# Kernel tuning notes

Hardware: AMD Instinct MI355X
Metric: run time of the kernel (lower is better)

The kernel has to match this reference:

```python
import jax, jax.numpy as jnp
import numpy as np

DIM = 2048
HEADS = 16
DIM_HEAD = 128
INNER = HEADS * DIM_HEAD  # 2048


def rotate_half(x):
    # split last dim into two halves, return cat(-x2, x1)
    x1, x2 = jnp.split(x, 2, axis=-1)
    return jnp.concatenate((-x2, x1), axis=-1)


def rotary_pos(n, dim_head, dtype):
    inv_freq = 1.0 / (10000.0 ** (jnp.arange(0, dim_head, 2, dtype=jnp.float32) / dim_head))
    seq = jnp.arange(n, dtype=jnp.float32)
    freqs = jnp.einsum('i,j->ij', seq, inv_freq)  # [n, dim_head//2]
    return jnp.concatenate((freqs, freqs), axis=-1).astype(dtype)  # [n, dim_head]


def apply_rotary(pos, t):
    return t * jnp.cos(pos) + rotate_half(t) * jnp.sin(pos)


def setup_inputs() -> dict:
    key = jax.random.key(0)
    ks = jax.random.split(key, 9)
    s = 0.02
    return {
        'x': jax.random.normal(ks[0], (2, 2048, DIM), dtype=jnp.float32),
        'Wq': jax.random.normal(ks[1], (DIM, INNER), dtype=jnp.float32) * s,
        'bq': jnp.zeros((INNER,), dtype=jnp.float32),
        'Wk': jax.random.normal(ks[2], (DIM, INNER), dtype=jnp.float32) * s,
        'bk': jnp.zeros((INNER,), dtype=jnp.float32),
        'Wv': jax.random.normal(ks[3], (DIM, INNER), dtype=jnp.float32) * s,
        'bv': jnp.zeros((INNER,), dtype=jnp.float32),
        'Wo': jax.random.normal(ks[4], (INNER, DIM), dtype=jnp.float32) * s,
        'bo': jnp.zeros((DIM,), dtype=jnp.float32),
    }


def reference(x, Wq, bq, Wk, bk, Wv, bv, Wo, bo):
    b, n, _ = x.shape
    scale = DIM_HEAD ** -0.5

    def proj(W, bias):
        t = x @ W + bias                       # [b, n, inner]
        return t.reshape(b, n, HEADS, DIM_HEAD).transpose(0, 2, 1, 3)  # [b, h, n, d]

    q = proj(Wq, bq) * scale
    k = proj(Wk, bk)
    v = proj(Wv, bv)

    pos = rotary_pos(n, DIM_HEAD, x.dtype)     # [n, d]
    q = apply_rotary(pos, q)
    k = apply_rotary(pos, k)

    sim = jnp.einsum('bhid,bhjd->bhij', q, k)  # [b, h, n, n]
    causal = jnp.triu(jnp.ones((n, n), dtype=bool), k=1)
    sim = jnp.where(causal, -jnp.finfo(sim.dtype).max, sim)
    attn = jax.nn.softmax(sim, axis=-1)

    out = jnp.einsum('bhij,bhjd->bhid', attn, v)
    out = out.transpose(0, 2, 1, 3).reshape(b, n, INNER)
    return out @ Wo + bo
```

## Files before the change

kernel.cpp:

```cpp
#include <hip/hip_runtime.h>
#include <stdint.h>

typedef unsigned short u16;
typedef __bf16 bf16x8 __attribute__((ext_vector_type(8)));
typedef float f32x4 __attribute__((ext_vector_type(4)));
typedef float f32x16 __attribute__((ext_vector_type(16)));
typedef unsigned short u16x8 __attribute__((ext_vector_type(8)));
typedef unsigned short u16x4 __attribute__((ext_vector_type(4)));

#define MFMA16(a, b, c) __builtin_amdgcn_mfma_f32_16x16x32_bf16(a, b, c, 0, 0, 0)
#define MFMA32(a, b, c) __builtin_amdgcn_mfma_f32_32x32x16_bf16(a, b, c, 0, 0, 0)

static __device__ __forceinline__ u16 f2bf(float f) {
  union { float f; uint32_t u; } v; v.f = f;
  uint32_t r = 0x7FFFu + ((v.u >> 16) & 1u);
  return (u16)((v.u + r) >> 16);
}
static __device__ __forceinline__ float bf2f(u16 h) {
  union { uint32_t u; float f; } v; v.u = ((uint32_t)h) << 16;
  return v.f;
}

static __device__ __forceinline__ void gld_lds16(const u16* g, u16* l) {
  __builtin_amdgcn_global_load_lds(
      (const __attribute__((address_space(1))) void*)g,
      (__attribute__((address_space(3))) void*)l, 16, 0, 0);
}

__global__ __launch_bounds__(256) void cast_f32_to_bf16(
    const float* __restrict__ in, u16* __restrict__ out, int n4) {
  int i = blockIdx.x * blockDim.x + threadIdx.x;
  if (i >= n4) return;
  const float4 v = ((const float4*)in)[i];
  u16x4 o;
  o[0] = f2bf(v.x); o[1] = f2bf(v.y); o[2] = f2bf(v.z); o[3] = f2bf(v.w);
  ((u16x4*)out)[i] = o;
}

__global__ __launch_bounds__(256) void transpose_cast(
    const float* __restrict__ W, u16* __restrict__ Wt, int R, int C) {
  __shared__ float tile[32][33];
  const int bx = blockIdx.x * 32;
  const int by = blockIdx.y * 32;
  const int tx = threadIdx.x & 31, ty = threadIdx.x >> 5;
#pragma unroll
  for (int i = 0; i < 32; i += 8)
    tile[ty + i][tx] = W[(long)(by + ty + i) * C + bx + tx];
  __syncthreads();
#pragma unroll
  for (int i = 0; i < 32; i += 8)
    Wt[(long)(bx + ty + i) * R + by + tx] = f2bf(tile[tx][ty + i]);
}

__global__ __launch_bounds__(256) void rope_kernel(
    u16* __restrict__ q, u16* __restrict__ k) {
  const int idx = blockIdx.x * blockDim.x + threadIdx.x;
  if (idx >= 4096 * 16 * 64) return;
  const int j = idx & 63;
  const int h = (idx >> 6) & 15;
  const int row = idx >> 10;
  const int npos = row & 2047;
  const float inv_freq = exp2f(-0.20762051f * (float)j);
  const float pos = (float)npos * inv_freq;
  float s, c;
  sincosf(pos, &s, &c);
  const float scale = 0.08838834764831845f;
  const long base = (long)row * 2048 + h * 128 + j;
  float q1 = bf2f(q[base]), q2 = bf2f(q[base + 64]);
  q[base]      = f2bf((q1 * c - q2 * s) * scale);
  q[base + 64] = f2bf((q2 * c + q1 * s) * scale);
  float k1 = bf2f(k[base]), k2 = bf2f(k[base + 64]);
  k[base]      = f2bf(k1 * c - k2 * s);
  k[base + 64] = f2bf(k2 * c + k1 * s);
}

template <int OUT_F32>
static __device__ __forceinline__ void gemm_tile(
    const u16* __restrict__ A, const u16* __restrict__ Bt,
    const float* __restrict__ bias, void* __restrict__ C,
    const int M, const int N, const int K,
    u16* As, u16* Bs, const int bx, const int by) {
  const int tid = threadIdx.x;
  const int wave = tid >> 6;
  const int lane = tid & 63;
  const int lr = lane & 15, hi = lane >> 4;
  const int row0 = by * 128, col0 = bx * 128;
  const int wr = (wave >> 1) * 64, wc = (wave & 1) * 64;

  const int srow = tid >> 2;
  const int scol = (tid & 3) * 8;
  const u16* gA0 = A + (long)(row0 + srow) * K + scol;
  const u16* gA1 = gA0 + (long)64 * K;
  const u16* gB0 = Bt + (long)(col0 + srow) * K + scol;
  const u16* gB1 = gB0 + (long)64 * K;
  u16* lA0 = As + wave * 512;
  u16* lA1 = As + 2048 + wave * 512;
  u16* lB0 = Bs + wave * 512;
  u16* lB1 = Bs + 2048 + wave * 512;

  f32x4 acc[4][4] = {};

  for (int k0 = 0; k0 < K; k0 += 32) {
    __syncthreads();
    gld_lds16(gA0 + k0, lA0);
    gld_lds16(gA1 + k0, lA1);
    gld_lds16(gB0 + k0, lB0);
    gld_lds16(gB1 + k0, lB1);
    __syncthreads();
    bf16x8 af[4], bfr[4];
#pragma unroll
    for (int m = 0; m < 4; ++m)
      af[m] = *(const bf16x8*)&As[(wr + m * 16 + lr) * 32 + hi * 8];
#pragma unroll
    for (int n = 0; n < 4; ++n)
      bfr[n] = *(const bf16x8*)&Bs[(wc + n * 16 + lr) * 32 + hi * 8];
#pragma unroll
    for (int m = 0; m < 4; ++m)
#pragma unroll
      for (int n = 0; n < 4; ++n)
        acc[m][n] = MFMA16(af[m], bfr[n], acc[m][n]);
  }

#pragma unroll
  for (int n = 0; n < 4; ++n) {
    const int gcol = col0 + wc + n * 16 + lr;
    const float bb = bias[gcol];
#pragma unroll
    for (int m = 0; m < 4; ++m) {
      const int grow = row0 + wr + m * 16 + 4 * hi;
#pragma unroll
      for (int i = 0; i < 4; ++i) {
        const float v = acc[m][n][i] + bb;
        if (OUT_F32)
          ((float*)C)[(long)(grow + i) * N + gcol] = v;
        else
          ((u16*)C)[(long)(grow + i) * N + gcol] = f2bf(v);
      }
    }
  }
}

__global__ __launch_bounds__(256, 2) void gemm_qkv_kernel(
    const u16* __restrict__ xb,
    const u16* __restrict__ wtq, const u16* __restrict__ wtk, const u16* __restrict__ wtv,
    const float* __restrict__ bq, const float* __restrict__ bk, const float* __restrict__ bv,
    u16* __restrict__ qo, u16* __restrict__ ko, u16* __restrict__ vo) {
  __shared__ u16 As[4096], Bs[4096];
  const u16* Bt; const float* bias; u16* C;
  if (blockIdx.z == 0)      { Bt = wtq; bias = bq; C = qo; }
  else if (blockIdx.z == 1) { Bt = wtk; bias = bk; C = ko; }
  else                      { Bt = wtv; bias = bv; C = vo; }
  gemm_tile<0>(xb, Bt, bias, C, 4096, 2048, 2048, As, Bs, blockIdx.x, blockIdx.y);
}

__global__ __launch_bounds__(256, 2) void gemm_out_kernel(
    const u16* __restrict__ ao, const u16* __restrict__ wto,
    const float* __restrict__ bo, float* __restrict__ out) {
  __shared__ u16 As[4096], Bs[4096];
  gemm_tile<1>(ao, wto, bo, out, 4096, 2048, 2048, As, Bs, blockIdx.x, blockIdx.y);
}

__global__ __launch_bounds__(256, 2) void flash_attn_kernel(
    const u16* __restrict__ Q, const u16* __restrict__ K,
    const u16* __restrict__ V, u16* __restrict__ O) {
  __shared__ u16 Ks[2][8192];
  __shared__ char Vs[2][16640];

  const int tid = threadIdx.x;
  const int w = tid >> 6;
  const int lane = tid & 63;
  const int l31 = lane & 31, hi5 = lane >> 5, l15 = lane & 15, bit4 = (lane >> 4) & 1;
  const int qt = 15 - blockIdx.x;
  const int q0 = qt * 128;
  const int bh = blockIdx.y;
  const long plane = (long)(bh >> 4) * 2048 * 2048 + (long)(bh & 15) * 128;
  const u16* Qb = Q + plane;
  const u16* Kb = K + plane;
  const u16* Vb = V + plane;
  const int qrow = q0 + w * 32 + l31;

  bf16x8 qf[8];
#pragma unroll
  for (int c = 0; c < 8; ++c)
    qf[c] = *(const bf16x8*)(Qb + (long)qrow * 2048 + c * 16 + hi5 * 8);

  int srcKoff[4], srcVoff[4];
#pragma unroll
  for (int cc = 0; cc < 4; ++cc) {
    const int ci = cc * 256 + tid;
    const int krow = ci >> 4;
    const int cL = (ci & 15) * 16;
    srcKoff[cc] = krow * 2048 + ((cL ^ ((krow & 15) << 4)) >> 1);
    const int dg16 = ci >> 7;
    const int w2 = ci & 127;
    srcVoff[cc] = (w2 >> 1) * 2048 + dg16 * 16 + (w2 & 1) * 8;
  }

  f32x16 ot[4] = {};
  float m = -3e38f, lp = 0.f;
  const int nkt = 2 * qt + 2;
  const int swzk = l15 << 4;
  const int vbase = bit4 * 2080 + hi5 * 256 + l15 * 8;

  auto STAGE = [&](int buf, int kt1) {
    const long koff = (long)kt1 * 131072;
#pragma unroll
    for (int cc = 0; cc < 4; ++cc) {
      gld_lds16(Kb + koff + srcKoff[cc], &Ks[buf][cc * 2048 + w * 512]);
      const int ci0 = cc * 256 + w * 64;
      gld_lds16(Vb + koff + srcVoff[cc],
                (u16*)&Vs[buf][(ci0 >> 7) * 2080 + (ci0 & 127) * 16]);
    }
  };

  STAGE(0, 0);
  for (int kt = 0; kt < nkt; ++kt) {
    __syncthreads();
    if (kt + 1 < nkt) STAGE((kt + 1) & 1, kt + 1);
    const int kv0 = kt * 64;
    if (kv0 > q0 + w * 32 + 31) continue;

    const char* KT = (const char*)Ks[kt & 1];
    const char* VT = Vs[kt & 1];

    f32x16 sa[2] = {};
#pragma unroll
    for (int g = 0; g < 2; ++g) {
      const int rowb = (g * 32 + l31) * 256;
#pragma unroll
      for (int c = 0; c < 8; ++c) {
        const int ab = rowb + ((c * 32 + hi5 * 16) ^ swzk);
        const bf16x8 kf = *(const bf16x8*)(KT + ab);
        sa[g] = MFMA32(kf, qf[c], sa[g]);
      }
    }

    if (kv0 + 63 > q0 + w * 32) {
#pragma unroll
      for (int g = 0; g < 2; ++g)
#pragma unroll
        for (int r = 0; r < 16; ++r) {
          const int kv = kv0 + g * 32 + (r & 3) + 8 * (r >> 2) + 4 * hi5;
          if (kv > qrow) sa[g][r] = -1e30f;
        }
    }

    float pm = -3e38f;
#pragma unroll
    for (int g = 0; g < 2; ++g)
#pragma unroll
      for (int r = 0; r < 16; ++r) pm = fmaxf(pm, sa[g][r]);
    pm = fmaxf(pm, __shfl_xor(pm, 32));
    const float mnew = fmaxf(m, pm);
    const float alpha = __expf(m - mnew);
    float psum = 0.f;
#pragma unroll
    for (int g = 0; g < 2; ++g)
#pragma unroll
      for (int r = 0; r < 16; ++r) {
        const float pv = __expf(sa[g][r] - mnew);
        sa[g][r] = pv;
        psum += pv;
      }
    lp = lp * alpha + psum;
    m = mnew;
#pragma unroll
    for (int dg = 0; dg < 4; ++dg) ot[dg] *= alpha;

    uint32_t pk[2][8];
#pragma unroll
    for (int g = 0; g < 2; ++g)
#pragma unroll
      for (int k2 = 0; k2 < 8; ++k2)
        asm("v_cvt_pk_bf16_f32 %0, %1, %2"
            : "=v"(pk[g][k2]) : "v"(sa[g][2 * k2]), "v"(sa[g][2 * k2 + 1]));

    bf16x8 pfrag[4];
#pragma unroll
    for (int kc = 0; kc < 4; ++kc) {
      const int g = kc >> 1, b = 4 * (kc & 1);
      const uint32_t lo0 = pk[g][b],     lo1 = pk[g][b + 1];
      const uint32_t hh0 = pk[g][b + 2], hh1 = pk[g][b + 3];
      const uint32_t s0v = hi5 ? lo0 : hh0;
      const uint32_t s1v = hi5 ? lo1 : hh1;
      const uint32_t r0 = (uint32_t)__shfl_xor((int)s0v, 32);
      const uint32_t r1 = (uint32_t)__shfl_xor((int)s1v, 32);
      union { uint32_t u[4]; bf16x8 v; } fu;
      fu.u[0] = hi5 ? r0 : lo0;
      fu.u[1] = hi5 ? r1 : lo1;
      fu.u[2] = hi5 ? hh0 : r0;
      fu.u[3] = hi5 ? hh1 : r1;
      pfrag[kc] = fu.v;
    }

#pragma unroll
    for (int dg = 0; dg < 4; ++dg) {
      unsigned long long t[8];
#pragma unroll
      for (int kc = 0; kc < 4; ++kc)
#pragma unroll
        for (int r = 0; r < 2; ++r) {
          const uint32_t a = (uint32_t)(size_t)VT + (uint32_t)(vbase + dg * 4160 + kc * 512 + r * 128);
          asm volatile("ds_read_b64_tr_b16 %0, %1" : "=v"(t[kc * 2 + r]) : "v"(a));
        }
      asm volatile("s_waitcnt lgkmcnt(0)" ::: "memory");
      __builtin_amdgcn_sched_barrier(0);
#pragma unroll
      for (int kc = 0; kc < 4; ++kc) {
        union { unsigned long long q[2]; bf16x8 v; } vu;
        vu.q[0] = t[kc * 2]; vu.q[1] = t[kc * 2 + 1];
        ot[dg] = MFMA32(vu.v, pfrag[kc], ot[dg]);
      }
    }
  }

  const float lt = lp + __shfl_xor(lp, 32);
  const float inv = 1.0f / lt;
  u16* Ob = (u16*)O + plane;
#pragma unroll
  for (int dg = 0; dg < 4; ++dg)
#pragma unroll
    for (int rq = 0; rq < 4; ++rq) {
      u16x4 pk4;
#pragma unroll
      for (int j = 0; j < 4; ++j) pk4[j] = f2bf(ot[dg][rq * 4 + j] * inv);
      *(u16x4*)(Ob + (long)qrow * 2048 + dg * 32 + 8 * rq + 4 * hi5) = pk4;
    }
}

extern "C" void kernel_launch(void* const* d_in, const int* in_sizes, int n_in,
                              void* d_out, int out_size, void* d_ws, size_t ws_size,
                              hipStream_t stream) {
  const float* x  = (const float*)d_in[0];
  const float* Wq = (const float*)d_in[1];
  const float* bq = (const float*)d_in[2];
  const float* Wk = (const float*)d_in[3];
  const float* bk = (const float*)d_in[4];
  const float* Wv = (const float*)d_in[5];
  const float* bv = (const float*)d_in[6];
  const float* Wo = (const float*)d_in[7];
  const float* bo = (const float*)d_in[8];
  float* out = (float*)d_out;

  char* ws = (char*)d_ws;
  size_t off = 0;
  u16* xb   = (u16*)(ws + off); off += (size_t)4096 * 2048 * 2;
  u16* wtq  = (u16*)(ws + off); off += (size_t)2048 * 2048 * 2;
  u16* wtk  = (u16*)(ws + off); off += (size_t)2048 * 2048 * 2;
  u16* wtv  = (u16*)(ws + off); off += (size_t)2048 * 2048 * 2;
  u16* wto  = (u16*)(ws + off); off += (size_t)2048 * 2048 * 2;
  u16* qlin = (u16*)(ws + off); off += (size_t)4096 * 2048 * 2;
  u16* klin = (u16*)(ws + off); off += (size_t)4096 * 2048 * 2;
  u16* vlin = (u16*)(ws + off); off += (size_t)4096 * 2048 * 2;
  u16* aout = (u16*)(ws + off); off += (size_t)4096 * 2048 * 2;
  (void)ws_size; (void)in_sizes; (void)n_in; (void)out_size;

  cast_f32_to_bf16<<<dim3(8192), dim3(256), 0, stream>>>(x, xb, 4096 * 2048 / 4);
  dim3 tgrid(64, 64);
  transpose_cast<<<tgrid, dim3(256), 0, stream>>>(Wq, wtq, 2048, 2048);
  transpose_cast<<<tgrid, dim3(256), 0, stream>>>(Wk, wtk, 2048, 2048);
  transpose_cast<<<tgrid, dim3(256), 0, stream>>>(Wv, wtv, 2048, 2048);
  transpose_cast<<<tgrid, dim3(256), 0, stream>>>(Wo, wto, 2048, 2048);

  gemm_qkv_kernel<<<dim3(16, 32, 3), dim3(256), 0, stream>>>(
      xb, wtq, wtk, wtv, bq, bk, bv, qlin, klin, vlin);
  rope_kernel<<<dim3(16384), dim3(256), 0, stream>>>(qlin, klin);
  flash_attn_kernel<<<dim3(16, 32), dim3(256), 0, stream>>>(qlin, klin, vlin, aout);
  gemm_out_kernel<<<dim3(16, 32), dim3(256), 0, stream>>>(aout, wto, bo, out);
}
```

Measured before the change: 434.5 us.

## Rewrite GEMM tiles as double-buffered 128x256 tiles with swizzled LDS and prefetch

Replaces the single-buffered 128x128, K=32 GEMM tile with a 512-thread 128x256 tile that steps K by 64. Global-to-LDS loads for the next step are issued while the current step's MFMAs run, with explicit vmcnt waits, barriers and setprio hints. The LDS layout is XOR-swizzled to avoid bank conflicts. The goal is to hide global-load latency and raise arithmetic intensity in the QKV and output projections, at the cost of much larger LDS use (96KB per block) and fewer blocks in flight.

```diff
diff --git a/kernel.cpp b/kernel.cpp
--- a/kernel.cpp
+++ b/kernel.cpp
@@ -75,59 +75,115 @@
 }
 
 template <int OUT_F32>
-static __device__ __forceinline__ void gemm_tile(
+static __device__ __forceinline__ void gemm_bigtile(
     const u16* __restrict__ A, const u16* __restrict__ Bt,
     const float* __restrict__ bias, void* __restrict__ C,
-    const int M, const int N, const int K,
     u16* As, u16* Bs, const int bx, const int by) {
+  constexpr int K = 2048, N = 2048;
   const int tid = threadIdx.x;
-  const int wave = tid >> 6;
-  const int lane = tid & 63;
-  const int lr = lane & 15, hi = lane >> 4;
-  const int row0 = by * 128, col0 = bx * 128;
-  const int wr = (wave >> 1) * 64, wc = (wave & 1) * 64;
-
-  const int srow = tid >> 2;
-  const int scol = (tid & 3) * 8;
-  const u16* gA0 = A + (long)(row0 + srow) * K + scol;
-  const u16* gA1 = gA0 + (long)64 * K;
-  const u16* gB0 = Bt + (long)(col0 + srow) * K + scol;
-  const u16* gB1 = gB0 + (long)64 * K;
-  u16* lA0 = As + wave * 512;
-  u16* lA1 = As + 2048 + wave * 512;
-  u16* lB0 = Bs + wave * 512;
-  u16* lB1 = Bs + 2048 + wave * 512;
+  const int w = tid >> 6, lane = tid & 63;
+  const int l15 = lane & 15, hi2 = lane >> 4;
+  const int wm = w >> 2, wn = w & 3;
+  const int row0 = by * 128, col0 = bx * 256;
+
+  const int cswz = (tid & 3) ^ ((tid >> 3) & 3);
+  const u16* srcA  = A + (long)(row0 + (tid >> 2)) * K + cswz * 8;
+  const u16* srcB0 = Bt + (long)(col0 + (tid >> 2)) * K + cswz * 8;
+  const u16* srcB1 = srcB0 + (long)128 * K;
+
+  int aoff[4], boff[4];
+#pragma unroll
+  for (int f = 0; f < 4; ++f) {
+    const int ra = wm * 64 + f * 16 + l15;
+    aoff[f] = ra * 64 + ((hi2 ^ ((ra >> 1) & 3)) << 4);
+    const int rb = wn * 64 + f * 16 + l15;
+    boff[f] = rb * 64 + ((hi2 ^ ((rb >> 1) & 3)) << 4);
+  }
+  const char* AsB = (const char*)As;
+  const char* BsB = (const char*)Bs;
 
   f32x4 acc[4][4] = {};
 
-  for (int k0 = 0; k0 < K; k0 += 32) {
-    __syncthreads();
-    gld_lds16(gA0 + k0, lA0);
-    gld_lds16(gA1 + k0, lA1);
-    gld_lds16(gB0 + k0, lB0);
-    gld_lds16(gB1 + k0, lB1);
-    __syncthreads();
+  {
+    gld_lds16(srcB0, Bs + w * 512);
+    gld_lds16(srcB1, Bs + 4096 + w * 512);
+    gld_lds16(srcB0 + 32, Bs + 8192 + w * 512);
+    gld_lds16(srcB1 + 32, Bs + 8192 + 4096 + w * 512);
+    gld_lds16(srcA, As + w * 512);
+    gld_lds16(srcA + 32, As + 4096 + w * 512);
+  }
+  asm volatile("s_waitcnt vmcnt(1)" ::: "memory");
+  __builtin_amdgcn_s_barrier();
+
+  constexpr int NT = K / 64;
+  for (int t = 0; t < NT - 1; ++t) {
+    const int buf = t & 1, nbuf = buf ^ 1;
+    const char* Ab = AsB + buf * 16384;
+    const char* Bb = BsB + buf * 32768;
+    const int g1 = (t + 1) * 64;
     bf16x8 af[4], bfr[4];
 #pragma unroll
+    for (int f = 0; f < 4; ++f) af[f] = *(const bf16x8*)(Ab + aoff[f]);
+#pragma unroll
+    for (int f = 0; f < 4; ++f) bfr[f] = *(const bf16x8*)(Bb + boff[f]);
+    gld_lds16(srcB0 + g1, Bs + nbuf * 16384 + w * 512);
+    gld_lds16(srcB1 + g1, Bs + nbuf * 16384 + 4096 + w * 512);
+    gld_lds16(srcB0 + g1 + 32, Bs + nbuf * 16384 + 8192 + w * 512);
+    gld_lds16(srcB1 + g1 + 32, Bs + nbuf * 16384 + 8192 + 4096 + w * 512);
+    asm volatile("s_waitcnt vmcnt(4)" ::: "memory");
+    __builtin_amdgcn_s_barrier();
+    __builtin_amdgcn_s_setprio(1);
+#pragma unroll
     for (int m = 0; m < 4; ++m)
-      af[m] = *(const bf16x8*)&As[(wr + m * 16 + lr) * 32 + hi * 8];
-#pragma unroll
-    for (int n = 0; n < 4; ++n)
-      bfr[n] = *(const bf16x8*)&Bs[(wc + n * 16 + lr) * 32 + hi * 8];
+#pragma unroll
+      for (int n = 0; n < 4; ++n) acc[m][n] = MFMA16(af[m], bfr[n], acc[m][n]);
+    __builtin_amdgcn_s_setprio(0);
+#pragma unroll
+    for (int f = 0; f < 4; ++f) af[f] = *(const bf16x8*)(Ab + 8192 + aoff[f]);
+#pragma unroll
+    for (int f = 0; f < 4; ++f) bfr[f] = *(const bf16x8*)(Bb + 16384 + boff[f]);
+    gld_lds16(srcA + g1, As + nbuf * 8192 + w * 512);
+    gld_lds16(srcA + g1 + 32, As + nbuf * 8192 + 4096 + w * 512);
+    asm volatile("s_waitcnt vmcnt(1)" ::: "memory");
+    __builtin_amdgcn_s_setprio(1);
 #pragma unroll
     for (int m = 0; m < 4; ++m)
 #pragma unroll
-      for (int n = 0; n < 4; ++n)
-        acc[m][n] = MFMA16(af[m], bfr[n], acc[m][n]);
+      for (int n = 0; n < 4; ++n) acc[m][n] = MFMA16(af[m], bfr[n], acc[m][n]);
+    __builtin_amdgcn_s_setprio(0);
+    __builtin_amdgcn_s_barrier();
+  }
+  {
+    const char* Ab = AsB + 16384;
+    const char* Bb = BsB + 32768;
+    bf16x8 af[4], bfr[4];
+#pragma unroll
+    for (int f = 0; f < 4; ++f) af[f] = *(const bf16x8*)(Ab + aoff[f]);
+#pragma unroll
+    for (int f = 0; f < 4; ++f) bfr[f] = *(const bf16x8*)(Bb + boff[f]);
+    asm volatile("s_waitcnt vmcnt(0)" ::: "memory");
+    __builtin_amdgcn_s_barrier();
+#pragma unroll
+    for (int m = 0; m < 4; ++m)
+#pragma unroll
+      for (int n = 0; n < 4; ++n) acc[m][n] = MFMA16(af[m], bfr[n], acc[m][n]);
+#pragma unroll
+    for (int f = 0; f < 4; ++f) af[f] = *(const bf16x8*)(Ab + 8192 + aoff[f]);
+#pragma unroll
+    for (int f = 0; f < 4; ++f) bfr[f] = *(const bf16x8*)(Bb + 16384 + boff[f]);
+#pragma unroll
+    for (int m = 0; m < 4; ++m)
+#pragma unroll
+      for (int n = 0; n < 4; ++n) acc[m][n] = MFMA16(af[m], bfr[n], acc[m][n]);
   }
 
 #pragma unroll
   for (int n = 0; n < 4; ++n) {
-    const int gcol = col0 + wc + n * 16 + lr;
+    const int gcol = col0 + wn * 64 + n * 16 + l15;
     const float bb = bias[gcol];
 #pragma unroll
     for (int m = 0; m < 4; ++m) {
-      const int grow = row0 + wr + m * 16 + 4 * hi;
+      const int grow = row0 + wm * 64 + m * 16 + 4 * hi2;
 #pragma unroll
       for (int i = 0; i < 4; ++i) {
         const float v = acc[m][n][i] + bb;
@@ -140,24 +196,24 @@
   }
 }
 
-__global__ __launch_bounds__(256, 2) void gemm_qkv_kernel(
+__global__ __launch_bounds__(512) void gemm_qkv_kernel(
     const u16* __restrict__ xb,
     const u16* __restrict__ wtq, const u16* __restrict__ wtk, const u16* __restrict__ wtv,
     const float* __restrict__ bq, const float* __restrict__ bk, const float* __restrict__ bv,
     u16* __restrict__ qo, u16* __restrict__ ko, u16* __restrict__ vo) {
-  __shared__ u16 As[4096], Bs[4096];
+  __shared__ u16 As[16384], Bs[32768];
   const u16* Bt; const float* bias; u16* C;
   if (blockIdx.z == 0)      { Bt = wtq; bias = bq; C = qo; }
   else if (blockIdx.z == 1) { Bt = wtk; bias = bk; C = ko; }
   else                      { Bt = wtv; bias = bv; C = vo; }
-  gemm_tile<0>(xb, Bt, bias, C, 4096, 2048, 2048, As, Bs, blockIdx.x, blockIdx.y);
-}
-
-__global__ __launch_bounds__(256, 2) void gemm_out_kernel(
+  gemm_bigtile<0>(xb, Bt, bias, C, As, Bs, blockIdx.x, blockIdx.y);
+}
+
+__global__ __launch_bounds__(512) void gemm_out_kernel(
     const u16* __restrict__ ao, const u16* __restrict__ wto,
     const float* __restrict__ bo, float* __restrict__ out) {
-  __shared__ u16 As[4096], Bs[4096];
-  gemm_tile<1>(ao, wto, bo, out, 4096, 2048, 2048, As, Bs, blockIdx.x, blockIdx.y);
+  __shared__ u16 As[16384], Bs[32768];
+  gemm_bigtile<1>(ao, wto, bo, out, As, Bs, blockIdx.x, blockIdx.y);
 }
 
 __global__ __launch_bounds__(256, 2) void flash_attn_kernel(
@@ -362,9 +418,9 @@
   transpose_cast<<<tgrid, dim3(256), 0, stream>>>(Wv, wtv, 2048, 2048);
   transpose_cast<<<tgrid, dim3(256), 0, stream>>>(Wo, wto, 2048, 2048);
 
-  gemm_qkv_kernel<<<dim3(16, 32, 3), dim3(256), 0, stream>>>(
+  gemm_qkv_kernel<<<dim3(8, 32, 3), dim3(512), 0, stream>>>(
       xb, wtq, wtk, wtv, bq, bk, bv, qlin, klin, vlin);
   rope_kernel<<<dim3(16384), dim3(256), 0, stream>>>(qlin, klin);
   flash_attn_kernel<<<dim3(16, 32), dim3(256), 0, stream>>>(qlin, klin, vlin, aout);
-  gemm_out_kernel<<<dim3(16, 32), dim3(256), 0, stream>>>(aout, wto, bo, out);
-}
+  gemm_out_kernel<<<dim3(8, 32), dim3(512), 0, stream>>>(aout, wto, bo, out);
+}
```

Result: no change. 442.7 us (+1.9%).

## Rewrite projection GEMMs with 256-row tiles, 4-stage async LDS pipeline, swizzle

Applied to the files above, without the earlier changes.

Replaces the 128x128 single-buffered GEMM tile with a 512-thread 256xBN tile (BN=256 for QKV, 128 for output projection). Global-to-LDS loads run through a 4-stage ring with explicit vmcnt waits, so loads for later k-steps overlap MFMA work on the current one. The change also adds an XOR swizzle to the LDS layout against bank conflicts, raises MFMA wave priority, and remaps block IDs for L2 locality. It uses far more LDS per block (up to 128KB), which limits occupancy, and it hardcodes K=N=2048.

```diff
diff --git a/kernel.cpp b/kernel.cpp
--- a/kernel.cpp
+++ b/kernel.cpp
@@ -74,63 +74,108 @@
   k[base + 64] = f2bf(k2 * c + k1 * s);
 }
 
-template <int OUT_F32>
-static __device__ __forceinline__ void gemm_tile(
+template <int OUT_F32, int BN>
+static __device__ __forceinline__ void gemm256(
     const u16* __restrict__ A, const u16* __restrict__ Bt,
     const float* __restrict__ bias, void* __restrict__ C,
-    const int M, const int N, const int K,
-    u16* As, u16* Bs, const int bx, const int by) {
+    char* ldsA, char* ldsB, const int bm, const int bn) {
+  constexpr int K = 2048, N = 2048, NT = 64;
+  constexpr int NF = BN / 64;
+  constexpr int NBI = BN / 128;
   const int tid = threadIdx.x;
-  const int wave = tid >> 6;
-  const int lane = tid & 63;
-  const int lr = lane & 15, hi = lane >> 4;
-  const int row0 = by * 128, col0 = bx * 128;
-  const int wr = (wave >> 1) * 64, wc = (wave & 1) * 64;
-
-  const int srow = tid >> 2;
-  const int scol = (tid & 3) * 8;
-  const u16* gA0 = A + (long)(row0 + srow) * K + scol;
-  const u16* gA1 = gA0 + (long)64 * K;
-  const u16* gB0 = Bt + (long)(col0 + srow) * K + scol;
-  const u16* gB1 = gB0 + (long)64 * K;
-  u16* lA0 = As + wave * 512;
-  u16* lA1 = As + 2048 + wave * 512;
-  u16* lB0 = Bs + wave * 512;
-  u16* lB1 = Bs + 2048 + wave * 512;
-
-  f32x4 acc[4][4] = {};
-
-  for (int k0 = 0; k0 < K; k0 += 32) {
-    __syncthreads();
-    gld_lds16(gA0 + k0, lA0);
-    gld_lds16(gA1 + k0, lA1);
-    gld_lds16(gB0 + k0, lB0);
-    gld_lds16(gB1 + k0, lB1);
-    __syncthreads();
-    bf16x8 af[4], bfr[4];
-#pragma unroll
-    for (int m = 0; m < 4; ++m)
-      af[m] = *(const bf16x8*)&As[(wr + m * 16 + lr) * 32 + hi * 8];
-#pragma unroll
-    for (int n = 0; n < 4; ++n)
-      bfr[n] = *(const bf16x8*)&Bs[(wc + n * 16 + lr) * 32 + hi * 8];
-#pragma unroll
-    for (int m = 0; m < 4; ++m)
-#pragma unroll
-      for (int n = 0; n < 4; ++n)
-        acc[m][n] = MFMA16(af[m], bfr[n], acc[m][n]);
-  }
-
-#pragma unroll
-  for (int n = 0; n < 4; ++n) {
-    const int gcol = col0 + wc + n * 16 + lr;
+  const int w = tid >> 6, lane = tid & 63;
+  const int l15 = lane & 15, hi2 = (lane >> 4) & 3;
+  const int wm = w >> 2, wn = w & 3;
+  const int row0 = bm * 256, col0 = bn * BN;
+
+  const int srcch = ((tid & 3) ^ ((tid >> 3) & 3)) * 8;
+  const u16* sA0 = A + (long)(row0 + (tid >> 2)) * K + srcch;
+  const u16* sA1 = sA0 + (long)128 * K;
+  const u16* sB0 = Bt + (long)(col0 + (tid >> 2)) * K + srcch;
+  const u16* sB1 = sB0 + (long)128 * K;
+
+  int aoff[8], boff[NF];
+#pragma unroll
+  for (int f = 0; f < 8; ++f) {
+    const int r = wm * 128 + f * 16 + l15;
+    aoff[f] = r * 64 + ((hi2 ^ ((r >> 1) & 3)) << 4);
+  }
+#pragma unroll
+  for (int n = 0; n < NF; ++n) {
+    const int r = wn * (BN / 4) + n * 16 + l15;
+    boff[n] = r * 64 + ((hi2 ^ ((r >> 1) & 3)) << 4);
+  }
+
+  f32x4 acc[8][NF] = {};
+
+  auto ISSUE = [&](int tt) {
+    const long kof = (long)tt * 32;
+    const int b = tt & 3;
+    u16* Ad = (u16*)(ldsA + b * 16384) + w * 512;
+    gld_lds16(sA0 + kof, Ad);
+    gld_lds16(sA1 + kof, Ad + 4096);
+    u16* Bd = (u16*)(ldsB + b * (NBI * 8192)) + w * 512;
+    gld_lds16(sB0 + kof, Bd);
+    if constexpr (NBI == 2) gld_lds16(sB1 + kof, Bd + 4096);
+  };
+
+  auto BODY = [&](int buf, bool issue, int tt) {
+    const char* Ab = ldsA + buf * 16384;
+    const char* Bb = ldsB + buf * (NBI * 8192);
+    bf16x8 af[8], bfr[NF];
+#pragma unroll
+    for (int f = 0; f < 8; ++f) af[f] = *(const bf16x8*)(Ab + aoff[f]);
+#pragma unroll
+    for (int n = 0; n < NF; ++n) bfr[n] = *(const bf16x8*)(Bb + boff[n]);
+    if (issue) ISSUE(tt);
+    __builtin_amdgcn_s_setprio(1);
+#pragma unroll
+    for (int f = 0; f < 8; ++f)
+#pragma unroll
+      for (int n = 0; n < NF; ++n) acc[f][n] = MFMA16(af[f], bfr[n], acc[f][n]);
+    __builtin_amdgcn_s_setprio(0);
+  };
+
+#define WAIT_MAIN()                                                        \
+  do {                                                                     \
+    if constexpr (BN == 256) asm volatile("s_waitcnt vmcnt(8)" ::: "memory"); \
+    else asm volatile("s_waitcnt vmcnt(6)" ::: "memory");                  \
+  } while (0)
+#define WAIT_HALF()                                                        \
+  do {                                                                     \
+    if constexpr (BN == 256) asm volatile("s_waitcnt vmcnt(4)" ::: "memory"); \
+    else asm volatile("s_waitcnt vmcnt(3)" ::: "memory");                  \
+  } while (0)
+#define BARSB()                     \
+  __builtin_amdgcn_s_barrier();     \
+  __builtin_amdgcn_sched_barrier(0)
+
+  ISSUE(0); ISSUE(1); ISSUE(2);
+
+#pragma unroll 4
+  for (int t = 0; t < NT - 4; ++t) {
+    WAIT_MAIN(); BARSB();
+    BODY(t & 3, true, t + 3);
+  }
+  WAIT_MAIN(); BARSB(); BODY(0, true, 63);
+  WAIT_MAIN(); BARSB(); BODY(1, false, 0);
+  WAIT_HALF(); BARSB(); BODY(2, false, 0);
+  asm volatile("s_waitcnt vmcnt(0)" ::: "memory");
+  BARSB(); BODY(3, false, 0);
+#undef WAIT_MAIN
+#undef WAIT_HALF
+#undef BARSB
+
+#pragma unroll
+  for (int n = 0; n < NF; ++n) {
+    const int gcol = col0 + wn * (BN / 4) + n * 16 + l15;
     const float bb = bias[gcol];
 #pragma unroll
-    for (int m = 0; m < 4; ++m) {
-      const int grow = row0 + wr + m * 16 + 4 * hi;
+    for (int f = 0; f < 8; ++f) {
+      const int grow = row0 + wm * 128 + f * 16 + 4 * hi2;
 #pragma unroll
       for (int i = 0; i < 4; ++i) {
-        const float v = acc[m][n][i] + bb;
+        const float v = acc[f][n][i] + bb;
         if (OUT_F32)
           ((float*)C)[(long)(grow + i) * N + gcol] = v;
         else
@@ -140,24 +185,30 @@
   }
 }
 
-__global__ __launch_bounds__(256, 2) void gemm_qkv_kernel(
+__global__ __launch_bounds__(512, 2) void gemm_qkv_kernel(
     const u16* __restrict__ xb,
     const u16* __restrict__ wtq, const u16* __restrict__ wtk, const u16* __restrict__ wtv,
     const float* __restrict__ bq, const float* __restrict__ bk, const float* __restrict__ bv,
     u16* __restrict__ qo, u16* __restrict__ ko, u16* __restrict__ vo) {
-  __shared__ u16 As[4096], Bs[4096];
+  __shared__ char ldsA[65536], ldsB[65536];
+  const int id = blockIdx.x;
+  const int swz = (id & 7) * 16 + (id >> 3);
+  const int bm = swz >> 3, bn = swz & 7;
   const u16* Bt; const float* bias; u16* C;
-  if (blockIdx.z == 0)      { Bt = wtq; bias = bq; C = qo; }
-  else if (blockIdx.z == 1) { Bt = wtk; bias = bk; C = ko; }
+  if (blockIdx.y == 0)      { Bt = wtq; bias = bq; C = qo; }
+  else if (blockIdx.y == 1) { Bt = wtk; bias = bk; C = ko; }
   else                      { Bt = wtv; bias = bv; C = vo; }
-  gemm_tile<0>(xb, Bt, bias, C, 4096, 2048, 2048, As, Bs, blockIdx.x, blockIdx.y);
-}
-
-__global__ __launch_bounds__(256, 2) void gemm_out_kernel(
+  gemm256<0, 256>(xb, Bt, bias, C, ldsA, ldsB, bm, bn);
+}
+
+__global__ __launch_bounds__(512, 2) void gemm_out_kernel(
     const u16* __restrict__ ao, const u16* __restrict__ wto,
     const float* __restrict__ bo, float* __restrict__ out) {
-  __shared__ u16 As[4096], Bs[4096];
-  gemm_tile<1>(ao, wto, bo, out, 4096, 2048, 2048, As, Bs, blockIdx.x, blockIdx.y);
+  __shared__ char ldsA[65536], ldsB[32768];
+  const int id = blockIdx.x;
+  const int swz = (id & 7) * 32 + (id >> 3);
+  const int bm = swz >> 4, bn = swz & 15;
+  gemm256<1, 128>(ao, wto, bo, out, ldsA, ldsB, bm, bn);
 }
 
 __global__ __launch_bounds__(256, 2) void flash_attn_kernel(
@@ -362,9 +413,9 @@
   transpose_cast<<<tgrid, dim3(256), 0, stream>>>(Wv, wtv, 2048, 2048);
   transpose_cast<<<tgrid, dim3(256), 0, stream>>>(Wo, wto, 2048, 2048);
 
-  gemm_qkv_kernel<<<dim3(16, 32, 3), dim3(256), 0, stream>>>(
+  gemm_qkv_kernel<<<dim3(128, 3), dim3(512), 0, stream>>>(
       xb, wtq, wtk, wtv, bq, bk, bv, qlin, klin, vlin);
   rope_kernel<<<dim3(16384), dim3(256), 0, stream>>>(qlin, klin);
   flash_attn_kernel<<<dim3(16, 32), dim3(256), 0, stream>>>(qlin, klin, vlin, aout);
-  gemm_out_kernel<<<dim3(16, 32), dim3(256), 0, stream>>>(aout, wto, bo, out);
-}
+  gemm_out_kernel<<<dim3(256), dim3(512), 0, stream>>>(aout, wto, bo, out);
+}
```

After: 420.0 us. 3.3% less time.
